# Performance work log

Measured on AMD Instinct MI355X. Metric: run time of the kernel, lower is better.

The kernel has to match this reference:

```python
import jax, jax.numpy as jnp
import numpy as np

D_MODEL, N_HEADS, D_HEAD, D_MLP = 768, 12, 64, 3072
BATCH, SEQ = 2, 2048
EPS = 1e-5
IGNORE = -100000.0
INIT = 0.02


def gelu_new(x):
    # GPT-2 tanh-approx GELU
    c = jnp.sqrt(2.0 / jnp.pi).astype(x.dtype)
    return 0.5 * x * (1.0 + jnp.tanh(c * (x + 0.044715 * x ** 3)))


def layer_norm(x, w, b):
    x = x - jnp.mean(x, axis=-1, keepdims=True)
    scale = jnp.sqrt(jnp.mean(x * x, axis=-1, keepdims=True) + EPS)
    return (x / scale) * w + b


def setup_inputs() -> dict:
    key = jax.random.key(0)
    ks = jax.random.split(key, 8)
    f32 = jnp.float32
    return {
        "resid_pre": jax.random.normal(ks[0], (BATCH, SEQ, D_MODEL), f32),
        "W_Q": INIT * jax.random.normal(ks[1], (N_HEADS, D_MODEL, D_HEAD), f32),
        "b_Q": jnp.zeros((N_HEADS, D_HEAD), f32),
        "W_K": INIT * jax.random.normal(ks[2], (N_HEADS, D_MODEL, D_HEAD), f32),
        "b_K": jnp.zeros((N_HEADS, D_HEAD), f32),
        "W_V": INIT * jax.random.normal(ks[3], (N_HEADS, D_MODEL, D_HEAD), f32),
        "b_V": jnp.zeros((N_HEADS, D_HEAD), f32),
        "W_O": INIT * jax.random.normal(ks[4], (N_HEADS, D_HEAD, D_MODEL), f32),
        "b_O": jnp.zeros((D_MODEL,), f32),
        "ln1_w": jnp.ones((D_MODEL,), f32),
        "ln1_b": jnp.zeros((D_MODEL,), f32),
        "ln2_w": jnp.ones((D_MODEL,), f32),
        "ln2_b": jnp.zeros((D_MODEL,), f32),
        "W_in": INIT * jax.random.normal(ks[5], (D_MODEL, D_MLP), f32),
        "b_in": jnp.zeros((D_MLP,), f32),
        "W_out": INIT * jax.random.normal(ks[6], (D_MLP, D_MODEL), f32),
        "b_out": jnp.zeros((D_MODEL,), f32),
    }


def reference(resid_pre, W_Q, b_Q, W_K, b_K, W_V, b_V, W_O, b_O,
              ln1_w, ln1_b, ln2_w, ln2_b, W_in, b_in, W_out, b_out):
    x = layer_norm(resid_pre, ln1_w, ln1_b)
    # per-head projections: [batch, pos, heads, d_head]
    q = jnp.einsum('bsd,hde->bshe', x, W_Q) + b_Q
    k = jnp.einsum('bsd,hde->bshe', x, W_K) + b_K
    v = jnp.einsum('bsd,hde->bshe', x, W_V) + b_V
    scores = jnp.einsum('bqhe,bkhe->bhqk', q, k) / jnp.sqrt(jnp.float32(D_HEAD))
    S = scores.shape[-1]
    causal = jnp.triu(jnp.ones((S, S), bool), k=1)
    scores = jnp.where(causal, jnp.float32(IGNORE), scores)
    pattern = jax.nn.softmax(scores, axis=-1)
    z = jnp.einsum('bhqk,bkhe->bqhe', pattern, v)
    attn_out = jnp.einsum('bqhe,hed->bqd', z, W_O) + b_O
    resid_mid = resid_pre + attn_out
    y = layer_norm(resid_mid, ln2_w, ln2_b)
    mlp_out = jnp.einsum('bsd,dm->bsm', y, W_in) + b_in
    mlp_out = gelu_new(mlp_out)
    mlp_out = jnp.einsum('bsm,md->bsd', mlp_out, W_out) + b_out
    return resid_mid + mlp_out
```

## Files before the change

### kernel.cpp

```cpp
#include <hip/hip_runtime.h>
#include <hip/hip_bf16.h>

#define SEQ   2048
#define DMODEL 768
#define NHEADS 12
#define DHEAD  64
#define DMLP  3072
#define TTOK  4096
#define EPSLN 1e-5f

typedef unsigned short u16;
typedef __attribute__((ext_vector_type(4))) float f32x4;
typedef __attribute__((ext_vector_type(8))) short s16x8;
typedef __attribute__((ext_vector_type(8))) unsigned short u16x8;
typedef __attribute__((ext_vector_type(4))) unsigned short u16x4;

__device__ __forceinline__ float bf2f(u16 u) {
    return __uint_as_float(((unsigned int)u) << 16);
}
__device__ __forceinline__ u16 f2bf(float f) {
    unsigned int x = __float_as_uint(f);
    return (u16)((x + 0x7FFFu + ((x >> 16) & 1u)) >> 16);
}
__device__ __forceinline__ bool is_bf16(const void* probe) {
    return ((const u16*)probe)[0] == 0x3F80u;
}
__device__ __forceinline__ float readIn(const void* p, long i, bool bf) {
    return bf ? bf2f(((const u16*)p)[i]) : ((const float*)p)[i];
}

__device__ __forceinline__ float gelu_new(float x) {
    float x3 = x * x * x;
    float u = 0.7978845608028654f * (x + 0.044715f * x3);
    return 0.5f * x * (1.0f + tanhf(u));
}

__device__ __forceinline__ void stage16(const u16* g, u16* l) {
    __builtin_amdgcn_global_load_lds(
        (const __attribute__((address_space(1))) void*)g,
        (__attribute__((address_space(3))) void*)l,
        16, 0, 0);
}

__global__ __launch_bounds__(256) void prologue_kernel(
    const void* W_O, const void* W_in, const void* W_out,
    const void* W_Q, const void* W_K, const void* W_V,
    const void* bq, const void* bk, const void* bv, const void* bo,
    const void* bin, const void* bout,
    const void* l1w, const void* l1b, const void* l2w, const void* l2b,
    const void* resid_pre,
    u16* __restrict__ WOT, u16* __restrict__ WinT, u16* __restrict__ WoutT,
    u16* __restrict__ WqkvT, u16* __restrict__ x_ln1,
    float* __restrict__ bias_qkv, float* __restrict__ bias_o,
    float* __restrict__ bias_in, float* __restrict__ bias_out, float* __restrict__ lnv)
{
    bool bf = is_bf16(l1w);
    int id = blockIdx.x;
    int tid = threadIdx.x;

    if (id >= 6913) {
        int t = id - 6913;
        __shared__ float red[8];
        float v[3];
#pragma unroll
        for (int j = 0; j < 3; j++)
            v[j] = readIn(resid_pre, (long)t * DMODEL + tid + j * 256, bf);
        float s = v[0] + v[1] + v[2];
#pragma unroll
        for (int off = 1; off < 64; off <<= 1) s += __shfl_xor(s, off, 64);
        if ((tid & 63) == 0) red[tid >> 6] = s;
        __syncthreads();
        float mean = (red[0] + red[1] + red[2] + red[3]) * (1.0f / DMODEL);
        float sq = 0.0f;
#pragma unroll
        for (int j = 0; j < 3; j++) { v[j] -= mean; sq += v[j] * v[j]; }
#pragma unroll
        for (int off = 1; off < 64; off <<= 1) sq += __shfl_xor(sq, off, 64);
        if ((tid & 63) == 0) red[4 + (tid >> 6)] = sq;
        __syncthreads();
        float var = (red[4] + red[5] + red[6] + red[7]) * (1.0f / DMODEL);
        float inv = rsqrtf(var + EPSLN);
#pragma unroll
        for (int j = 0; j < 3; j++) {
            int c = tid + j * 256;
            x_ln1[(size_t)t * DMODEL + c] =
                f2bf(v[j] * inv * readIn(l1w, c, bf) + readIn(l1b, c, bf));
        }
        return;
    }
    if (id == 6912) {
        for (int i = tid; i < 768; i += 256) {
            bias_qkv[i]        = readIn(bq, i, bf);
            bias_qkv[768 + i]  = readIn(bk, i, bf);
            bias_qkv[1536 + i] = readIn(bv, i, bf);
            bias_o[i]   = readIn(bo, i, bf);
            bias_out[i] = readIn(bout, i, bf);
            lnv[i]       = readIn(l2w, i, bf);
            lnv[768 + i] = readIn(l2b, i, bf);
        }
        for (int i = tid; i < 3072; i += 256) bias_in[i] = readIn(bin, i, bf);
        return;
    }
    const void* src; u16* dst; int R, C, tr, tc;
    size_t srcOff = 0, dstOff = 0;
    if (id < 576)       { src = W_O;  dst = WOT;  R = 768;  C = 768;  tr = id / 24;  tc = id % 24; }
    else if (id < 2880) { int j = id - 576;  src = W_in;  dst = WinT;  R = 768;  C = 3072; tr = j / 96; tc = j % 96; }
    else if (id < 5184) { int j = id - 2880; src = W_out; dst = WoutT; R = 3072; C = 768;  tr = j / 24; tc = j % 24; }
    else {
        int j = id - 5184;
        int q = j / 576, rem = j % 576, h = rem / 48, t = rem % 48;
        src = (q == 0) ? W_Q : (q == 1) ? W_K : W_V;
        dst = WqkvT; R = 768; C = 64; tr = t / 2; tc = t % 2;
        srcOff = (size_t)h * 49152;
        dstOff = ((size_t)q * 768 + h * 64) * 768;
    }
    __shared__ float tb[32][33];
    int tx = tid & 31, ty = tid >> 5;
    int r0 = tr * 32, c0 = tc * 32;
#pragma unroll
    for (int i = 0; i < 4; i++)
        tb[ty + i * 8][tx] = readIn(src, srcOff + (size_t)(r0 + ty + i * 8) * C + c0 + tx, bf);
    __syncthreads();
#pragma unroll
    for (int i = 0; i < 4; i++)
        dst[dstOff + (size_t)(c0 + ty + i * 8) * R + r0 + tx] = f2bf(tb[tx][ty + i * 8]);
}

__global__ __launch_bounds__(256) void ln_kernel(
    const u16* __restrict__ in, const float* __restrict__ w, const float* __restrict__ b,
    u16* __restrict__ out)
{
    int t = blockIdx.x;
    int tid = threadIdx.x;
    __shared__ float red[8];
    float v[3];
#pragma unroll
    for (int j = 0; j < 3; j++) v[j] = bf2f(in[(size_t)t * DMODEL + tid + j * 256]);
    float s = v[0] + v[1] + v[2];
#pragma unroll
    for (int off = 1; off < 64; off <<= 1) s += __shfl_xor(s, off, 64);
    if ((tid & 63) == 0) red[tid >> 6] = s;
    __syncthreads();
    float mean = (red[0] + red[1] + red[2] + red[3]) * (1.0f / DMODEL);
    float sq = 0.0f;
#pragma unroll
    for (int j = 0; j < 3; j++) { v[j] -= mean; sq += v[j] * v[j]; }
#pragma unroll
    for (int off = 1; off < 64; off <<= 1) sq += __shfl_xor(sq, off, 64);
    if ((tid & 63) == 0) red[4 + (tid >> 6)] = sq;
    __syncthreads();
    float var = (red[4] + red[5] + red[6] + red[7]) * (1.0f / DMODEL);
    float inv = rsqrtf(var + EPSLN);
#pragma unroll
    for (int j = 0; j < 3; j++) {
        int c = tid + j * 256;
        out[(size_t)t * DMODEL + c] = f2bf(v[j] * inv * w[c] + b[c]);
    }
}

template <int EPI, int BM, int BN>
__global__ __launch_bounds__(256) void mfma_gemm(
    const u16* __restrict__ A, const u16* __restrict__ Bt,
    const float* __restrict__ bias, const void* __restrict__ res,
    void* __restrict__ Cout, u16* __restrict__ Cout2,
    int M, int N, int K, const void* probe)
{
    constexpr int NI = BM / 32;
    constexpr int NJ = BN / 32;
    __shared__ u16 As[8][BM][8];
    __shared__ u16 Bs[8][BN][8];
    int tid = threadIdx.x, lane = tid & 63, w = tid >> 6;
    int nct = N / BN;
    int id = blockIdx.x;
    int sg = id / (8 * nct), rem = id % (8 * nct);
    int m0 = (sg * 8 + rem / nct) * BM;
    int n0 = (rem % nct) * BN;
    int wr = (w & 1) * (BM / 2), wc = (w >> 1) * (BN / 2);
    int lm = lane & 15, quad = lane >> 4;

    const u16* gA = A  + (size_t)(m0 + lane) * K;
    const u16* gB = Bt + (size_t)(n0 + lane) * K;
    size_t rowK64 = (size_t)64 * K;

    f32x4 acc[NI][NJ];
    const f32x4 z4 = {0.f, 0.f, 0.f, 0.f};
#pragma unroll
    for (int i = 0; i < NI; i++)
#pragma unroll
        for (int j = 0; j < NJ; j++) acc[i][j] = z4;

    for (int k0 = 0; k0 < K; k0 += 64) {
        stage16(gA + k0 + w * 8,       &As[w][0][0]);
        stage16(gA + k0 + (w + 4) * 8, &As[w + 4][0][0]);
        if (BM == 128) {
            stage16(gA + rowK64 + k0 + w * 8,       &As[w][64][0]);
            stage16(gA + rowK64 + k0 + (w + 4) * 8, &As[w + 4][64][0]);
        }
        stage16(gB + k0 + w * 8,       &Bs[w][0][0]);
        stage16(gB + k0 + (w + 4) * 8, &Bs[w + 4][0][0]);
        if (BN == 128) {
            stage16(gB + rowK64 + k0 + w * 8,       &Bs[w][64][0]);
            stage16(gB + rowK64 + k0 + (w + 4) * 8, &Bs[w + 4][64][0]);
        }
        __syncthreads();
#pragma unroll
        for (int c2 = 0; c2 < 2; c2++) {
            s16x8 af[NI], bfr[NJ];
#pragma unroll
            for (int i = 0; i < NI; i++)
                af[i] = *(const s16x8*)&As[c2 * 4 + quad][wr + i * 16 + lm][0];
#pragma unroll
            for (int j = 0; j < NJ; j++)
                bfr[j] = *(const s16x8*)&Bs[c2 * 4 + quad][wc + j * 16 + lm][0];
#pragma unroll
            for (int i = 0; i < NI; i++)
#pragma unroll
                for (int j = 0; j < NJ; j++)
                    acc[i][j] = __builtin_amdgcn_mfma_f32_16x16x32_bf16(
                        af[i], bfr[j], acc[i][j], 0, 0, 0);
        }
        __syncthreads();
    }

    bool pbf = (EPI == 2 || EPI == 3) ? is_bf16(probe) : false;
#pragma unroll
    for (int i = 0; i < NI; i++) {
#pragma unroll
        for (int j = 0; j < NJ; j++) {
            int col = n0 + wc + j * 16 + lm;
            float bsv = bias[col];
            int row0 = m0 + wr + i * 16 + quad * 4;
            if (EPI == 4) {
                if (col < 1536) {
#pragma unroll
                    for (int r = 0; r < 4; r++)
                        ((u16*)Cout)[(size_t)(row0 + r) * 1536 + col] = f2bf(acc[i][j][r] + bsv);
                } else {
                    int e9 = col - 1536, hh = e9 >> 6, ee = e9 & 63;
                    int bb = row0 >> 11, t0 = row0 & 2047;
                    u16x4 pv;
#pragma unroll
                    for (int r = 0; r < 4; r++) pv[r] = f2bf(acc[i][j][r] + bsv);
                    *(u16x4*)&Cout2[(((size_t)bb * 12 + hh) * 64 + ee) * 2048 + t0] = pv;
                }
            } else {
#pragma unroll
                for (int r = 0; r < 4; r++) {
                    size_t idx = (size_t)(row0 + r) * N + col;
                    float c = acc[i][j][r] + bsv;
                    if (EPI == 1) c = gelu_new(c);
                    if (EPI == 2) c += readIn(res, (long)idx, pbf);
                    if (EPI == 3) c += bf2f(((const u16*)res)[idx]);
                    if (EPI == 3) {
                        if (pbf) ((u16*)Cout)[idx] = f2bf(c);
                        else     ((float*)Cout)[idx] = c;
                    } else {
                        ((u16*)Cout)[idx] = f2bf(c);
                    }
                }
            }
        }
    }
}

__global__ __launch_bounds__(256) void attn_mfma(
    const u16* __restrict__ qk, const u16* __restrict__ vT, u16* __restrict__ z)
{
    __shared__ u16 Ps[4][16][40];

    int tid = threadIdx.x, lane = tid & 63, w = tid >> 6;
    int lm = lane & 15, quad = lane >> 4;
    int bh = blockIdx.x % 24;
    int qt = 31 - blockIdx.x / 24;
    int b = bh / 12, h = bh % 12;
    int q0 = qt * 64 + w * 16;

    const u16* qrow = qk + ((size_t)(b * SEQ) + q0 + lm) * 1536 + h * 64 + quad * 8;
    s16x8 aq0 = *(const s16x8*)(qrow);
    s16x8 aq1 = *(const s16x8*)(qrow + 32);

    const u16* kbase = qk + (size_t)(b * SEQ) * 1536 + 768 + h * 64 + quad * 8;
    const u16* vbase = vT + (size_t)bh * 64 * SEQ;

    f32x4 oacc[4], lacc;
    const f32x4 z4 = {0.f, 0.f, 0.f, 0.f};
#pragma unroll
    for (int g = 0; g < 4; g++) oacc[g] = z4;
    lacc = z4;
    s16x8 ones;
#pragma unroll
    for (int i = 0; i < 8; i++) ones[i] = (short)0x3F80;

    int ngroups = (q0 + 15) / 32 + 1;
    for (int kt = 0; kt < ngroups; kt++) {
        int k0 = kt * 32;
        const u16* kr = kbase + (size_t)(k0 + lm) * 1536;
        s16x8 bk00 = *(const s16x8*)(kr);
        s16x8 bk01 = *(const s16x8*)(kr + 32);
        const u16* kr1 = kr + (size_t)16 * 1536;
        s16x8 bk10 = *(const s16x8*)(kr1);
        s16x8 bk11 = *(const s16x8*)(kr1 + 32);
        s16x8 bv[4];
#pragma unroll
        for (int g = 0; g < 4; g++)
            bv[g] = *(const s16x8*)(vbase + (size_t)(g * 16 + lm) * SEQ + k0 + quad * 8);

        f32x4 s0 = __builtin_amdgcn_mfma_f32_16x16x32_bf16(aq0, bk00, z4, 0, 0, 0);
        s0 = __builtin_amdgcn_mfma_f32_16x16x32_bf16(aq1, bk01, s0, 0, 0, 0);
        f32x4 s1 = __builtin_amdgcn_mfma_f32_16x16x32_bf16(aq0, bk10, z4, 0, 0, 0);
        s1 = __builtin_amdgcn_mfma_f32_16x16x32_bf16(aq1, bk11, s1, 0, 0, 0);

#pragma unroll
        for (int r = 0; r < 4; r++) {
            int qr = q0 + quad * 4 + r;
            float p0 = (k0 + lm <= qr)      ? __expf(s0[r] * 0.125f) : 0.f;
            float p1 = (k0 + 16 + lm <= qr) ? __expf(s1[r] * 0.125f) : 0.f;
            Ps[w][quad * 4 + r][lm]      = f2bf(p0);
            Ps[w][quad * 4 + r][16 + lm] = f2bf(p1);
        }
        s16x8 ap = *(const s16x8*)&Ps[w][lm][quad * 8];

        lacc = __builtin_amdgcn_mfma_f32_16x16x32_bf16(ap, ones, lacc, 0, 0, 0);
#pragma unroll
        for (int g = 0; g < 4; g++)
            oacc[g] = __builtin_amdgcn_mfma_f32_16x16x32_bf16(ap, bv[g], oacc[g], 0, 0, 0);
    }

#pragma unroll
    for (int r = 0; r < 4; r++) {
        float inv = 1.0f / lacc[r];
        size_t row = (size_t)(b * SEQ) + q0 + quad * 4 + r;
#pragma unroll
        for (int g = 0; g < 4; g++)
            z[row * DMODEL + h * 64 + g * 16 + lm] = f2bf(oacc[g][r] * inv);
    }
}

extern "C" void kernel_launch(void* const* d_in, const int* in_sizes, int n_in,
                              void* d_out, int out_size, void* d_ws, size_t ws_size,
                              hipStream_t stream)
{
    const void* resid_pre = d_in[0];
    const void* W_Q = d_in[1];  const void* b_Q = d_in[2];
    const void* W_K = d_in[3];  const void* b_K = d_in[4];
    const void* W_V = d_in[5];  const void* b_V = d_in[6];
    const void* W_O = d_in[7];  const void* b_O = d_in[8];
    const void* ln1_w = d_in[9];  const void* ln1_b = d_in[10];
    const void* ln2_w = d_in[11]; const void* ln2_b = d_in[12];
    const void* W_in = d_in[13];  const void* b_in = d_in[14];
    const void* W_out = d_in[15]; const void* b_out = d_in[16];

    float* ws = (float*)d_ws;
    u16* qk        = (u16*)(ws);
    u16* vT        = (u16*)(ws + 3145728);
    u16* x_ln1     = (u16*)(ws + 4718592);
    u16* h_mlp     = (u16*)(ws);
    u16* z_buf     = (u16*)(ws + 6291456);
    u16* y_ln2     = z_buf;
    u16* resid_mid = (u16*)(ws + 7864320);
    u16* WqkvT     = (u16*)(ws + 9437184);
    u16* WOT       = (u16*)(ws + 10321920);
    u16* WinT      = (u16*)(ws + 10616832);
    u16* WoutT     = (u16*)(ws + 11796480);
    float* bias_qkv = ws + 12976128;
    float* bias_o   = ws + 12978432;
    float* bias_in  = ws + 12979200;
    float* bias_out = ws + 12982272;
    float* lnv      = ws + 12983040;

    prologue_kernel<<<6913 + TTOK, 256, 0, stream>>>(
        W_O, W_in, W_out, W_Q, W_K, W_V,
        b_Q, b_K, b_V, b_O, b_in, b_out,
        ln1_w, ln1_b, ln2_w, ln2_b, resid_pre,
        WOT, WinT, WoutT, WqkvT, x_ln1,
        bias_qkv, bias_o, bias_in, bias_out, lnv);
    mfma_gemm<4, 64, 128><<<1152, 256, 0, stream>>>(
        x_ln1, WqkvT, bias_qkv, nullptr, qk, vT, TTOK, 2304, DMODEL, nullptr);
    attn_mfma<<<768, 256, 0, stream>>>(qk, vT, z_buf);
    mfma_gemm<2, 64, 64><<<768, 256, 0, stream>>>(
        z_buf, WOT, bias_o, resid_pre, resid_mid, nullptr, TTOK, DMODEL, DMODEL, ln1_w);
    ln_kernel<<<TTOK, 256, 0, stream>>>(resid_mid, lnv, lnv + 768, y_ln2);
    mfma_gemm<1, 128, 128><<<768, 256, 0, stream>>>(
        y_ln2, WinT, bias_in, nullptr, h_mlp, nullptr, TTOK, DMLP, DMODEL, nullptr);
    mfma_gemm<3, 64, 64><<<768, 256, 0, stream>>>(
        h_mlp, WoutT, bias_out, resid_mid, d_out, nullptr, TTOK, DMODEL, DMLP, ln1_w);
}
```

Measured before the change: 443.2 us.

## Double-buffer GEMM k-tiles and stage attention K/V through shared memory

The GEMM main loop now uses 32-wide k-steps with two shared-memory buffers, so the next tile is staged while MFMAs run on the current one, and the loop keeps one barrier per step. The attention kernel now loads 64-key K and V^T tiles cooperatively into double-buffered LDS and register-prefetches the next tile, where before each wave read K/V straight from global memory. Causal masking is applied only on the diagonal tile. This aims to cut redundant global loads across waves and to hide memory latency, at the cost of more LDS use and more barriers per iteration.

```diff
diff --git a/kernel.cpp b/kernel.cpp
--- a/kernel.cpp
+++ b/kernel.cpp
@@ -167,8 +167,8 @@
 {
     constexpr int NI = BM / 32;
     constexpr int NJ = BN / 32;
-    __shared__ u16 As[8][BM][8];
-    __shared__ u16 Bs[8][BN][8];
+    __shared__ u16 As[2][4][BM][8];
+    __shared__ u16 Bs[2][4][BN][8];
     int tid = threadIdx.x, lane = tid & 63, w = tid >> 6;
     int nct = N / BN;
     int id = blockIdx.x;
@@ -189,36 +189,33 @@
 #pragma unroll
         for (int j = 0; j < NJ; j++) acc[i][j] = z4;
 
-    for (int k0 = 0; k0 < K; k0 += 64) {
-        stage16(gA + k0 + w * 8,       &As[w][0][0]);
-        stage16(gA + k0 + (w + 4) * 8, &As[w + 4][0][0]);
-        if (BM == 128) {
-            stage16(gA + rowK64 + k0 + w * 8,       &As[w][64][0]);
-            stage16(gA + rowK64 + k0 + (w + 4) * 8, &As[w + 4][64][0]);
-        }
-        stage16(gB + k0 + w * 8,       &Bs[w][0][0]);
-        stage16(gB + k0 + (w + 4) * 8, &Bs[w + 4][0][0]);
-        if (BN == 128) {
-            stage16(gB + rowK64 + k0 + w * 8,       &Bs[w][64][0]);
-            stage16(gB + rowK64 + k0 + (w + 4) * 8, &Bs[w + 4][64][0]);
-        }
-        __syncthreads();
-#pragma unroll
-        for (int c2 = 0; c2 < 2; c2++) {
-            s16x8 af[NI], bfr[NJ];
-#pragma unroll
-            for (int i = 0; i < NI; i++)
-                af[i] = *(const s16x8*)&As[c2 * 4 + quad][wr + i * 16 + lm][0];
+    auto stage = [&](int k0, int buf) {
+        stage16(gA + k0 + w * 8, &As[buf][w][0][0]);
+        if (BM == 128) stage16(gA + rowK64 + k0 + w * 8, &As[buf][w][64][0]);
+        stage16(gB + k0 + w * 8, &Bs[buf][w][0][0]);
+        if (BN == 128) stage16(gB + rowK64 + k0 + w * 8, &Bs[buf][w][64][0]);
+    };
+
+    stage(0, 0);
+    __syncthreads();
+    int nk = K >> 5;
+    for (int ki = 0; ki < nk; ki++) {
+        int cur = ki & 1;
+        if (ki + 1 < nk) stage((ki + 1) << 5, cur ^ 1);
+
+        s16x8 af[NI], bfr[NJ];
+#pragma unroll
+        for (int i = 0; i < NI; i++)
+            af[i] = *(const s16x8*)&As[cur][quad][wr + i * 16 + lm][0];
+#pragma unroll
+        for (int j = 0; j < NJ; j++)
+            bfr[j] = *(const s16x8*)&Bs[cur][quad][wc + j * 16 + lm][0];
+#pragma unroll
+        for (int i = 0; i < NI; i++)
 #pragma unroll
             for (int j = 0; j < NJ; j++)
-                bfr[j] = *(const s16x8*)&Bs[c2 * 4 + quad][wc + j * 16 + lm][0];
-#pragma unroll
-            for (int i = 0; i < NI; i++)
-#pragma unroll
-                for (int j = 0; j < NJ; j++)
-                    acc[i][j] = __builtin_amdgcn_mfma_f32_16x16x32_bf16(
-                        af[i], bfr[j], acc[i][j], 0, 0, 0);
-        }
+                acc[i][j] = __builtin_amdgcn_mfma_f32_16x16x32_bf16(
+                    af[i], bfr[j], acc[i][j], 0, 0, 0);
         __syncthreads();
     }
 
@@ -266,21 +263,35 @@
 __global__ __launch_bounds__(256) void attn_mfma(
     const u16* __restrict__ qk, const u16* __restrict__ vT, u16* __restrict__ z)
 {
-    __shared__ u16 Ps[4][16][40];
+    __shared__ u16 Ks[2][64][72];
+    __shared__ u16 Vt[2][64][72];
+    __shared__ u16 Ps[4][16][72];
 
     int tid = threadIdx.x, lane = tid & 63, w = tid >> 6;
     int lm = lane & 15, quad = lane >> 4;
     int bh = blockIdx.x % 24;
     int qt = 31 - blockIdx.x / 24;
     int b = bh / 12, h = bh % 12;
-    int q0 = qt * 64 + w * 16;
-
-    const u16* qrow = qk + ((size_t)(b * SEQ) + q0 + lm) * 1536 + h * 64 + quad * 8;
+    int q0 = qt * 64;
+
+    int tr = tid >> 2, tcg = (tid & 3) * 16;
+    const u16* qbase = qk + (size_t)(b * SEQ) * 1536 + h * 64;
+    const u16* kbase = qbase + 768;
+    const u16* vbase = vT + (size_t)bh * 64 * SEQ;
+
+    const u16* qrow = qbase + (size_t)(q0 + w * 16 + lm) * 1536 + quad * 8;
     s16x8 aq0 = *(const s16x8*)(qrow);
     s16x8 aq1 = *(const s16x8*)(qrow + 32);
 
-    const u16* kbase = qk + (size_t)(b * SEQ) * 1536 + 768 + h * 64 + quad * 8;
-    const u16* vbase = vT + (size_t)bh * 64 * SEQ;
+    {
+        const u16* gk = kbase + (size_t)tr * 1536 + tcg;
+        *(u16x8*)&Ks[0][tr][tcg]     = *(const u16x8*)gk;
+        *(u16x8*)&Ks[0][tr][tcg + 8] = *(const u16x8*)(gk + 8);
+        const u16* gv = vbase + (size_t)tr * SEQ + tcg;
+        *(u16x8*)&Vt[0][tr][tcg]     = *(const u16x8*)gv;
+        *(u16x8*)&Vt[0][tr][tcg + 8] = *(const u16x8*)(gv + 8);
+    }
+    __syncthreads();
 
     f32x4 oacc[4], lacc;
     const f32x4 z4 = {0.f, 0.f, 0.f, 0.f};
@@ -291,45 +302,70 @@
 #pragma unroll
     for (int i = 0; i < 8; i++) ones[i] = (short)0x3F80;
 
-    int ngroups = (q0 + 15) / 32 + 1;
-    for (int kt = 0; kt < ngroups; kt++) {
-        int k0 = kt * 32;
-        const u16* kr = kbase + (size_t)(k0 + lm) * 1536;
-        s16x8 bk00 = *(const s16x8*)(kr);
-        s16x8 bk01 = *(const s16x8*)(kr + 32);
-        const u16* kr1 = kr + (size_t)16 * 1536;
-        s16x8 bk10 = *(const s16x8*)(kr1);
-        s16x8 bk11 = *(const s16x8*)(kr1 + 32);
-        s16x8 bv[4];
-#pragma unroll
-        for (int g = 0; g < 4; g++)
-            bv[g] = *(const s16x8*)(vbase + (size_t)(g * 16 + lm) * SEQ + k0 + quad * 8);
-
-        f32x4 s0 = __builtin_amdgcn_mfma_f32_16x16x32_bf16(aq0, bk00, z4, 0, 0, 0);
-        s0 = __builtin_amdgcn_mfma_f32_16x16x32_bf16(aq1, bk01, s0, 0, 0, 0);
-        f32x4 s1 = __builtin_amdgcn_mfma_f32_16x16x32_bf16(aq0, bk10, z4, 0, 0, 0);
-        s1 = __builtin_amdgcn_mfma_f32_16x16x32_bf16(aq1, bk11, s1, 0, 0, 0);
-
-#pragma unroll
-        for (int r = 0; r < 4; r++) {
-            int qr = q0 + quad * 4 + r;
-            float p0 = (k0 + lm <= qr)      ? __expf(s0[r] * 0.125f) : 0.f;
-            float p1 = (k0 + 16 + lm <= qr) ? __expf(s1[r] * 0.125f) : 0.f;
-            Ps[w][quad * 4 + r][lm]      = f2bf(p0);
-            Ps[w][quad * 4 + r][16 + lm] = f2bf(p1);
-        }
-        s16x8 ap = *(const s16x8*)&Ps[w][lm][quad * 8];
-
-        lacc = __builtin_amdgcn_mfma_f32_16x16x32_bf16(ap, ones, lacc, 0, 0, 0);
-#pragma unroll
-        for (int g = 0; g < 4; g++)
-            oacc[g] = __builtin_amdgcn_mfma_f32_16x16x32_bf16(ap, bv[g], oacc[g], 0, 0, 0);
+    for (int kt = 0; kt <= qt; kt++) {
+        int cur = kt & 1;
+        u16x8 nk0, nk1, nv0, nv1;
+        bool pf = (kt < qt);
+        if (pf) {
+            int k0n = (kt + 1) * 64;
+            const u16* gk = kbase + (size_t)(k0n + tr) * 1536 + tcg;
+            nk0 = *(const u16x8*)gk;  nk1 = *(const u16x8*)(gk + 8);
+            const u16* gv = vbase + (size_t)tr * SEQ + k0n + tcg;
+            nv0 = *(const u16x8*)gv;  nv1 = *(const u16x8*)(gv + 8);
+        }
+
+        f32x4 sv[4];
+#pragma unroll
+        for (int g = 0; g < 4; g++) {
+            s16x8 bk0 = *(const s16x8*)&Ks[cur][g * 16 + lm][quad * 8];
+            s16x8 bk1 = *(const s16x8*)&Ks[cur][g * 16 + lm][32 + quad * 8];
+            f32x4 t = __builtin_amdgcn_mfma_f32_16x16x32_bf16(aq0, bk0, z4, 0, 0, 0);
+            sv[g] = __builtin_amdgcn_mfma_f32_16x16x32_bf16(aq1, bk1, t, 0, 0, 0);
+        }
+
+        if (kt == qt) {
+#pragma unroll
+            for (int g = 0; g < 4; g++)
+#pragma unroll
+                for (int r = 0; r < 4; r++) {
+                    bool ok = (g * 16 + lm) <= (w * 16 + quad * 4 + r);
+                    Ps[w][quad * 4 + r][g * 16 + lm] =
+                        ok ? f2bf(__expf(sv[g][r] * 0.125f)) : (u16)0;
+                }
+        } else {
+#pragma unroll
+            for (int g = 0; g < 4; g++)
+#pragma unroll
+                for (int r = 0; r < 4; r++)
+                    Ps[w][quad * 4 + r][g * 16 + lm] = f2bf(__expf(sv[g][r] * 0.125f));
+        }
+
+        s16x8 ap0 = *(const s16x8*)&Ps[w][lm][quad * 8];
+        s16x8 ap1 = *(const s16x8*)&Ps[w][lm][32 + quad * 8];
+
+        lacc = __builtin_amdgcn_mfma_f32_16x16x32_bf16(ap0, ones, lacc, 0, 0, 0);
+        lacc = __builtin_amdgcn_mfma_f32_16x16x32_bf16(ap1, ones, lacc, 0, 0, 0);
+#pragma unroll
+        for (int g = 0; g < 4; g++) {
+            s16x8 bv0 = *(const s16x8*)&Vt[cur][g * 16 + lm][quad * 8];
+            s16x8 bv1 = *(const s16x8*)&Vt[cur][g * 16 + lm][32 + quad * 8];
+            oacc[g] = __builtin_amdgcn_mfma_f32_16x16x32_bf16(ap0, bv0, oacc[g], 0, 0, 0);
+            oacc[g] = __builtin_amdgcn_mfma_f32_16x16x32_bf16(ap1, bv1, oacc[g], 0, 0, 0);
+        }
+
+        if (pf) {
+            *(u16x8*)&Ks[cur ^ 1][tr][tcg]     = nk0;
+            *(u16x8*)&Ks[cur ^ 1][tr][tcg + 8] = nk1;
+            *(u16x8*)&Vt[cur ^ 1][tr][tcg]     = nv0;
+            *(u16x8*)&Vt[cur ^ 1][tr][tcg + 8] = nv1;
+        }
+        __syncthreads();
     }
 
 #pragma unroll
     for (int r = 0; r < 4; r++) {
         float inv = 1.0f / lacc[r];
-        size_t row = (size_t)(b * SEQ) + q0 + quad * 4 + r;
+        size_t row = (size_t)(b * SEQ) + q0 + w * 16 + quad * 4 + r;
 #pragma unroll
         for (int g = 0; g < 4; g++)
             z[row * DMODEL + h * 64 + g * 16 + lm] = f2bf(oacc[g][r] * inv);
```

Result: faster. 375.4 us (-15.3%).
